# Optimization experiments

Hardware: AMD Instinct MI355X
Metric: run time of the kernel (lower is better)

Reference implementation:

```python
import jax, jax.numpy as jnp
import numpy as np

V, C, D = 131072, 65536, 128
E_NEG, E_CON = 131072, 524288
L, B = 3, 32


def setup_inputs() -> dict:
    key = jax.random.key(0)
    ks = jax.random.split(key, 16)
    s = 1.0 / np.sqrt(D)
    return {
        "x_var": jax.random.normal(ks[0], (V, D), jnp.float32),
        "x_con": jax.random.normal(ks[1], (C, D), jnp.float32),
        "W_src": jax.random.normal(ks[2], (L, 3, D, D), jnp.float32) * s,
        "W_dst": jax.random.normal(ks[3], (L, 3, D, D), jnp.float32) * s,
        "att_src": jax.random.normal(ks[4], (L, 3, D), jnp.float32) * s,
        "att_dst": jax.random.normal(ks[5], (L, 3, D), jnp.float32) * s,
        "bias": jnp.zeros((L, 3, D), jnp.float32),
        "mlp_w1": jax.random.normal(ks[6], (D, D), jnp.float32) * s,
        "mlp_b1": jnp.zeros((D,), jnp.float32),
        "mlp_w2": jax.random.normal(ks[7], (D, 1), jnp.float32) * s,
        "mlp_b2": jnp.zeros((1,), jnp.float32),
        "edge_neg_src": jax.random.randint(ks[8], (E_NEG,), 0, V, jnp.int32),
        "edge_neg_dst": jax.random.randint(ks[9], (E_NEG,), 0, V, jnp.int32),
        "edge_con_src": jax.random.randint(ks[10], (E_CON,), 0, V, jnp.int32),
        "edge_con_dst": jax.random.randint(ks[11], (E_CON,), 0, C, jnp.int32),
        "batch_var": jnp.sort(jax.random.randint(ks[12], (V,), 0, B, jnp.int32)),
    }


def _gat(xs, xd, src, dst, Ws, Wd, a_s, a_d, b, n_dst):
    """PyG GATConv (heads=1, add_self_loops=False) for one bipartite relation."""
    hs = xs @ Ws                                    # [Ns, D]
    hd = xd @ Wd                                    # [Nd, D]
    es = hs @ a_s                                   # [Ns]
    ed = hd @ a_d                                   # [Nd]
    e = jax.nn.leaky_relu(es[src] + ed[dst], negative_slope=0.2)  # [E]
    m = jax.ops.segment_max(e, dst, num_segments=n_dst)
    m = jnp.where(jnp.isfinite(m), m, 0.0)
    ex = jnp.exp(e - m[dst])
    den = jax.ops.segment_sum(ex, dst, num_segments=n_dst)
    alpha = ex / (den[dst] + 1e-16)                 # per-destination softmax
    out = jax.ops.segment_sum(hs[src] * alpha[:, None], dst, num_segments=n_dst)
    return out + b


def reference(x_var, x_con, W_src, W_dst, att_src, att_dst, bias,
              mlp_w1, mlp_b1, mlp_w2, mlp_b2,
              edge_neg_src, edge_neg_dst, edge_con_src, edge_con_dst, batch_var):
    xv, xc = x_var, x_con
    n_layers = W_src.shape[0]
    for l in range(n_layers):
        # relation 0: variable -is_negation_of-> variable
        v_neg = _gat(xv, xv, edge_neg_src, edge_neg_dst,
                     W_src[l, 0], W_dst[l, 0], att_src[l, 0], att_dst[l, 0], bias[l, 0], V)
        # relation 2: constraint -rev_connected_to-> variable (reverse edges)
        v_rev = _gat(xc, xv, edge_con_dst, edge_con_src,
                     W_src[l, 2], W_dst[l, 2], att_src[l, 2], att_dst[l, 2], bias[l, 2], V)
        # relation 1: variable -connected_to-> constraint
        c_new = _gat(xv, xc, edge_con_src, edge_con_dst,
                     W_src[l, 1], W_dst[l, 1], att_src[l, 1], att_dst[l, 1], bias[l, 1], C)
        # HeteroConv aggr='sum', then relu (dropout is identity in eval)
        xv = jax.nn.relu(v_neg + v_rev)
        xc = jax.nn.relu(c_new)
    # global_mean_pool over variable nodes per graph
    cnt = jax.ops.segment_sum(jnp.ones((V,), xv.dtype), batch_var, num_segments=B)
    pooled = jax.ops.segment_sum(xv, batch_var, num_segments=B) / jnp.maximum(cnt, 1.0)[:, None]
    # vote MLP: Linear -> relu -> Linear
    h = jax.nn.relu(pooled @ mlp_w1 + mlp_b1)
    return h @ mlp_w2 + mlp_b2
```

## Files before the change

### kernel.cpp

```cpp
#include <hip/hip_runtime.h>
#include <hip/hip_bf16.h>
#include <cstdint>
#include <cstddef>

#define D 128

typedef __hip_bfloat16 bf16;
typedef __attribute__((ext_vector_type(8))) short short8v;
typedef __attribute__((ext_vector_type(4))) float f32x4;

__device__ inline float ld1(const float* p) { return *p; }
__device__ inline float ld1(const bf16* p) { return __bfloat162float(*p); }
__device__ inline float2 ld2(const float* p) { return *(const float2*)p; }
__device__ inline float2 ld2(const bf16* p) {
  __hip_bfloat162 v = *(const __hip_bfloat162*)p;
  float2 r; r.x = __bfloat162float(v.x); r.y = __bfloat162float(v.y); return r;
}
__device__ inline void st2(float* p, float a, float b) {
  float2 v; v.x = a; v.y = b; *(float2*)p = v;
}
__device__ inline void st2(bf16* p, float a, float b) {
  __hip_bfloat162 v; v.x = __float2bfloat16(a); v.y = __float2bfloat16(b);
  *(__hip_bfloat162*)p = v;
}

__device__ inline short f2bf(float x) {
  uint32_t u = __builtin_bit_cast(uint32_t, x);
  uint32_t r = (u + 0x7FFFu + ((u >> 16) & 1u)) >> 16;
  return (short)(uint16_t)r;
}
__device__ inline float bf2f(short s) {
  uint32_t u = ((uint32_t)(uint16_t)s) << 16;
  return __builtin_bit_cast(float, u);
}

__device__ inline f32x4 mfma16(short8v a, short8v b, f32x4 c) {
  return __builtin_amdgcn_mfma_f32_16x16x32_bf16(a, b, c, 0, 0, 0);
}

__device__ __forceinline__ void load8(const float* p, float* v) {
  float4 a = *(const float4*)p;
  float4 b = *(const float4*)(p + 4);
  v[0] = a.x; v[1] = a.y; v[2] = a.z; v[3] = a.w;
  v[4] = b.x; v[5] = b.y; v[6] = b.z; v[7] = b.w;
}
__device__ __forceinline__ void load8(const bf16* p, float* v) {
  short8v s = *(const short8v*)p;
  #pragma unroll
  for (int j = 0; j < 8; ++j) v[j] = bf2f(s[j]);
}
__device__ __forceinline__ void split_store(short* Xh, short* Xl, int off, const float* v) {
  short8v h, l;
  #pragma unroll
  for (int j = 0; j < 8; ++j) {
    short hj = f2bf(v[j]);
    h[j] = hj;
    l[j] = f2bf(v[j] - bf2f(hj));
  }
  *(short8v*)&Xh[off] = h;
  *(short8v*)&Xl[off] = l;
}

__global__ void compute_u_kernel(const float* __restrict__ Wsrc, const float* __restrict__ Wdst,
                                 const float* __restrict__ asrc, const float* __restrict__ adst,
                                 float* __restrict__ u) {
  int lr = blockIdx.x;
  int side = blockIdx.y;
  int k = threadIdx.x;
  const float* W = (side == 0 ? Wsrc : Wdst) + ((size_t)lr * D + k) * D;
  const float* a = (side == 0 ? asrc : adst) + (size_t)lr * D;
  float s = 0.f;
  for (int j = 0; j < D; ++j) s += W[j] * a[j];
  u[((size_t)lr * 2 + side) * D + k] = s;
}

__global__ void wsplit_kernel(const float* __restrict__ Wsrc,
                              short* __restrict__ WhT, short* __restrict__ WlT) {
  int lr = blockIdx.x;
  const float* W = Wsrc + (size_t)lr * D * D;
  short* wh = WhT + (size_t)lr * D * D;
  short* wl = WlT + (size_t)lr * D * D;
  for (int i = threadIdx.x; i < D * D; i += blockDim.x) {
    int k = i >> 7, c = i & 127;
    float w = W[i];
    short h = f2bf(w);
    short l = f2bf(w - bf2f(h));
    wh[c * D + k] = h;
    wl[c * D + k] = l;
  }
}

__global__ void count_kernel(const int* __restrict__ dst, int* __restrict__ cnt, int E) {
  int i = blockIdx.x * blockDim.x + threadIdx.x;
  if (i < E) atomicAdd(&cnt[dst[i]], 1);
}

__global__ void count2_kernel(const int* __restrict__ csrc, const int* __restrict__ cdst,
                              int* __restrict__ cnt_bycon, int* __restrict__ cnt_byvar, int E) {
  int i = blockIdx.x * blockDim.x + threadIdx.x;
  if (i < E) {
    atomicAdd(&cnt_bycon[cdst[i]], 1);
    atomicAdd(&cnt_byvar[csrc[i]], 1);
  }
}

__global__ void bsum3_kernel(const int* __restrict__ c0, const int* __restrict__ c1,
                             const int* __restrict__ c2, int* __restrict__ bsums,
                             int n0, int n1, int n2, int pb0, int pb1, int pb2) {
  __shared__ int red[256];
  int y = blockIdx.y;
  const int* cnt = (y == 0) ? c0 : (y == 1) ? c1 : c2;
  int n  = (y == 0) ? n0 : (y == 1) ? n1 : n2;
  int pb = (y == 0) ? pb0 : (y == 1) ? pb1 : pb2;
  int b = blockIdx.x, t = threadIdx.x;
  int base = b * pb;
  if (base >= n) return;
  int end = base + pb; if (end > n) end = n;
  int s = 0;
  for (int i = base + t; i < end; i += 256) s += cnt[i];
  red[t] = s;
  __syncthreads();
  #pragma unroll
  for (int off = 128; off; off >>= 1) {
    if (t < off) red[t] += red[t + off];
    __syncthreads();
  }
  if (t == 0) bsums[y * 1024 + b] = red[0];
}

__global__ void bscan3_kernel(int* __restrict__ bsums,
                              int* __restrict__ t0, int* __restrict__ t1, int* __restrict__ t2) {
  __shared__ int sh[1024];
  int y = blockIdx.x, t = threadIdx.x;
  int* bs = bsums + y * 1024;
  int v = bs[t];
  sh[t] = v;
  __syncthreads();
  for (int off = 1; off < 1024; off <<= 1) {
    int u = (t >= off) ? sh[t - off] : 0;
    __syncthreads();
    sh[t] += u;
    __syncthreads();
  }
  bs[t] = sh[t] - v;
  if (t == 1023) {
    int* tot = (y == 0) ? t0 : (y == 1) ? t1 : t2;
    *tot = sh[1023];
  }
}

__global__ void scanfill3_kernel(const int* __restrict__ c0, const int* __restrict__ c1,
                                 const int* __restrict__ c2, const int* __restrict__ bsums,
                                 int* __restrict__ rp0, int* __restrict__ rp1, int* __restrict__ rp2,
                                 int* __restrict__ cu0, int* __restrict__ cu1, int* __restrict__ cu2,
                                 int n0, int n1, int n2, int pb0, int pb1, int pb2) {
  __shared__ int sh[256];
  int y = blockIdx.y;
  const int* cnt = (y == 0) ? c0 : (y == 1) ? c1 : c2;
  int* rowptr    = (y == 0) ? rp0 : (y == 1) ? rp1 : rp2;
  int* cursor    = (y == 0) ? cu0 : (y == 1) ? cu1 : cu2;
  int n  = (y == 0) ? n0 : (y == 1) ? n1 : n2;
  int pb = (y == 0) ? pb0 : (y == 1) ? pb1 : pb2;
  int b = blockIdx.x, t = threadIdx.x;
  int base = b * pb;
  if (base >= n) return;
  int end = base + pb; if (end > n) end = n;
  int run = bsums[y * 1024 + b];
  for (int tile = base; tile < end; tile += 256) {
    int i = tile + t;
    int c = (i < end) ? cnt[i] : 0;
    __syncthreads();
    sh[t] = c;
    __syncthreads();
    for (int off = 1; off < 256; off <<= 1) {
      int u = (t >= off) ? sh[t - off] : 0;
      __syncthreads();
      sh[t] += u;
      __syncthreads();
    }
    int excl = sh[t] - c;
    if (i < end) {
      rowptr[i] = run + excl;
      cursor[i] = run + excl;
    }
    run += sh[255];
  }
}

__global__ void fill_kernel(const int* __restrict__ dst, const int* __restrict__ src,
                            int* __restrict__ cursor, int* __restrict__ col, int E) {
  int i = blockIdx.x * blockDim.x + threadIdx.x;
  if (i < E) {
    int p = atomicAdd(&cursor[dst[i]], 1);
    col[p] = src[i];
  }
}

__global__ void fill2_kernel(const int* __restrict__ csrc, const int* __restrict__ cdst,
                             int* __restrict__ cur_bycon, int* __restrict__ cur_byvar,
                             int* __restrict__ col_bycon, int* __restrict__ col_byvar, int E) {
  int i = blockIdx.x * blockDim.x + threadIdx.x;
  if (i < E) {
    int s = csrc[i], d = cdst[i];
    int p = atomicAdd(&cur_bycon[d], 1);
    col_bycon[p] = s;
    int q = atomicAdd(&cur_byvar[s], 1);
    col_byvar[q] = d;
  }
}

template<typename T>
__global__ void vec_all_kernel(const T* __restrict__ xv, const T* __restrict__ xc,
                               const float* __restrict__ uv0, const float* __restrict__ uv1,
                               const float* __restrict__ uv2, const float* __restrict__ uv3,
                               const float* __restrict__ uc0, const float* __restrict__ uc1,
                               float* __restrict__ es0, float* __restrict__ ed0,
                               float* __restrict__ es1, float* __restrict__ ed2,
                               float* __restrict__ es2, float* __restrict__ ed1,
                               int V, int C) {
  int gw = (int)(((size_t)blockIdx.x * blockDim.x + threadIdx.x) >> 6);
  int lane = threadIdx.x & 63;
  if (gw < V) {
    const T* xr = xv + (size_t)gw * D;
    float xa = ld1(&xr[lane]), xb = ld1(&xr[lane + 64]);
    float p0 = xa * uv0[lane] + xb * uv0[lane + 64];
    float p1 = xa * uv1[lane] + xb * uv1[lane + 64];
    float p2 = xa * uv2[lane] + xb * uv2[lane + 64];
    float p3 = xa * uv3[lane] + xb * uv3[lane + 64];
    #pragma unroll
    for (int off = 32; off; off >>= 1) {
      p0 += __shfl_xor(p0, off);
      p1 += __shfl_xor(p1, off);
      p2 += __shfl_xor(p2, off);
      p3 += __shfl_xor(p3, off);
    }
    if (lane == 0) { es0[gw] = p0; ed0[gw] = p1; es1[gw] = p2; ed2[gw] = p3; }
  } else if (gw < V + C) {
    int g = gw - V;
    const T* xr = xc + (size_t)g * D;
    float xa = ld1(&xr[lane]), xb = ld1(&xr[lane + 64]);
    float p0 = xa * uc0[lane] + xb * uc0[lane + 64];
    float p1 = xa * uc1[lane] + xb * uc1[lane + 64];
    #pragma unroll
    for (int off = 32; off; off >>= 1) {
      p0 += __shfl_xor(p0, off);
      p1 += __shfl_xor(p1, off);
    }
    if (lane == 0) { es2[g] = p0; ed1[g] = p1; }
  }
}

template<typename Tin>
__global__ __launch_bounds__(512) void mm3_kernel(
    const Tin* __restrict__ Xv, const Tin* __restrict__ Xc,
    const short* __restrict__ wh0, const short* __restrict__ wl0,
    const short* __restrict__ wh1, const short* __restrict__ wl1,
    const short* __restrict__ wh2, const short* __restrict__ wl2,
    bf16* __restrict__ H0, bf16* __restrict__ H1, bf16* __restrict__ H2,
    int V, int C, int b0, int b1, int b2) {
  __shared__ short sbuf[2][2][32 * 136];
  int bid = blockIdx.x;
  const Tin* X; const short* wh; const short* wl; bf16* H;
  int nrows, lb, nblk;
  if (bid < b0)      { X = Xv; wh = wh0; wl = wl0; H = H0; nrows = V; lb = bid;      nblk = b0; }
  else if (bid < b1) { X = Xv; wh = wh1; wl = wl1; H = H1; nrows = V; lb = bid - b0; nblk = b1 - b0; }
  else               { X = Xc; wh = wh2; wl = wl2; H = H2; nrows = C; lb = bid - b1; nblk = b2 - b1; }
  int nchunks = nrows >> 5;
  if (lb >= nchunks) return;

  int tid = threadIdx.x;
  int wv = tid >> 6, lane = tid & 63;
  int c15 = lane & 15, q = lane >> 4;
  int rowgrp = wv >> 2, colgrp = wv & 3;

  short8v Bh[2][4], Bl[2][4];
  #pragma unroll
  for (int t = 0; t < 2; ++t) {
    #pragma unroll
    for (int ks = 0; ks < 4; ++ks) {
      int o = (colgrp * 32 + t * 16 + c15) * D + ks * 32 + q * 8;
      Bh[t][ks] = *(const short8v*)&wh[o];
      Bl[t][ks] = *(const short8v*)&wl[o];
    }
  }

  int srow = tid >> 4;
  int scol = (tid & 15) * 8;
  int soff = srow * 136 + scol;

  {
    float v[8];
    int gr = lb * 32 + srow; if (gr >= nrows) gr = nrows - 1;
    load8(X + (size_t)gr * D + scol, v);
    split_store(&sbuf[0][0][0], &sbuf[0][1][0], soff, v);
  }
  __syncthreads();

  int aoff = (rowgrp * 16 + c15) * 136 + q * 8;
  int cur = 0;
  for (int chunk = lb; chunk < nchunks; chunk += nblk) {
    int nxt = chunk + nblk;
    bool have = nxt < nchunks;
    float v[8];
    if (have) {
      int gr = nxt * 32 + srow; if (gr >= nrows) gr = nrows - 1;
      load8(X + (size_t)gr * D + scol, v);
    }
    const short* Ah = &sbuf[cur][0][aoff];
    const short* Al = &sbuf[cur][1][aoff];
    f32x4 a0 = (f32x4){0.f, 0.f, 0.f, 0.f};
    f32x4 a1 = (f32x4){0.f, 0.f, 0.f, 0.f};
    #pragma unroll
    for (int ks = 0; ks < 4; ++ks) {
      short8v xh = *(const short8v*)(Ah + ks * 32);
      short8v xl = *(const short8v*)(Al + ks * 32);
      a0 = mfma16(Bh[0][ks], xh, a0);
      a1 = mfma16(Bh[1][ks], xh, a1);
      a0 = mfma16(Bl[0][ks], xh, a0);
      a1 = mfma16(Bl[1][ks], xh, a1);
      a0 = mfma16(Bh[0][ks], xl, a0);
      a1 = mfma16(Bh[1][ks], xl, a1);
    }
    int gr = chunk * 32 + rowgrp * 16 + c15;
    if (gr < nrows) {
      short4 o0, o1;
      o0.x = f2bf(a0[0]); o0.y = f2bf(a0[1]); o0.z = f2bf(a0[2]); o0.w = f2bf(a0[3]);
      o1.x = f2bf(a1[0]); o1.y = f2bf(a1[1]); o1.z = f2bf(a1[2]); o1.w = f2bf(a1[3]);
      size_t base = (size_t)gr * D + colgrp * 32 + q * 4;
      *(short4*)((short*)H + base) = o0;
      *(short4*)((short*)H + base + 16) = o1;
    }
    if (have) split_store(&sbuf[cur ^ 1][0][0], &sbuf[cur ^ 1][1][0], soff, v);
    __syncthreads();
    cur ^= 1;
  }
}

__device__ __forceinline__ void alpha_rel(const int* __restrict__ rp, const int* __restrict__ col,
                                          const float* __restrict__ es, float edst,
                                          int gw, int lane, int2* __restrict__ edata) {
  int p0 = rp[gw];
  int deg = rp[gw + 1] - p0;
  if (deg <= 0) return;
  if (deg <= 64) {
    int s = 0; float e = -3.0e38f;
    if (lane < deg) {
      s = col[p0 + lane];
      float t = es[s] + edst;
      e = t > 0.f ? t : 0.2f * t;
    }
    float m = e;
    #pragma unroll
    for (int off = 32; off; off >>= 1) m = fmaxf(m, __shfl_xor(m, off));
    float ex = (lane < deg) ? __expf(e - m) : 0.f;
    float den = ex;
    #pragma unroll
    for (int off = 32; off; off >>= 1) den += __shfl_xor(den, off);
    float al = ex / (den + 1e-16f);
    if (lane < deg) {
      int2 v; v.x = s; v.y = __builtin_bit_cast(int, al);
      edata[p0 + lane] = v;
    }
  } else {
    float m = -3.0e38f;
    for (int j = lane; j < deg; j += 64) {
      int s = col[p0 + j];
      float t = es[s] + edst;
      t = t > 0.f ? t : 0.2f * t;
      m = fmaxf(m, t);
    }
    #pragma unroll
    for (int off = 32; off; off >>= 1) m = fmaxf(m, __shfl_xor(m, off));
    float den = 0.f;
    for (int j = lane; j < deg; j += 64) {
      int s = col[p0 + j];
      float t = es[s] + edst;
      t = t > 0.f ? t : 0.2f * t;
      den += __expf(t - m);
    }
    #pragma unroll
    for (int off = 32; off; off >>= 1) den += __shfl_xor(den, off);
    float inv = 1.f / (den + 1e-16f);
    for (int j = lane; j < deg; j += 64) {
      int s = col[p0 + j];
      float t = es[s] + edst;
      t = t > 0.f ? t : 0.2f * t;
      int2 v; v.x = s; v.y = __builtin_bit_cast(int, __expf(t - m) * inv);
      edata[p0 + j] = v;
    }
  }
}

__global__ void alpha_all_kernel(const int* __restrict__ rp0, const int* __restrict__ col0,
                                 const float* __restrict__ es0, const float* __restrict__ ed0,
                                 int2* __restrict__ eda0,
                                 const int* __restrict__ rp2, const int* __restrict__ col2,
                                 const float* __restrict__ es2, const float* __restrict__ ed2,
                                 int2* __restrict__ eda2,
                                 const int* __restrict__ rp1, const int* __restrict__ col1,
                                 const float* __restrict__ es1, const float* __restrict__ ed1,
                                 int2* __restrict__ eda1,
                                 int V, int C) {
  int gw = (int)(((size_t)blockIdx.x * blockDim.x + threadIdx.x) >> 6);
  int lane = threadIdx.x & 63;
  if (gw < V) {
    alpha_rel(rp0, col0, es0, ed0[gw], gw, lane, eda0);
    alpha_rel(rp2, col2, es2, ed2[gw], gw, lane, eda2);
  } else if (gw < V + C) {
    int g = gw - V;
    alpha_rel(rp1, col1, es1, ed1[g], g, lane, eda1);
  }
}

__device__ __forceinline__ void agg_rel(const int2* __restrict__ edata, int p0, int p1,
                                        const bf16* __restrict__ hs, int l2,
                                        float& a0, float& a1) {
  int q = p0;
  while (q + 4 <= p1) {
    int2 e0 = edata[q], e1 = edata[q + 1], e2 = edata[q + 2], e3 = edata[q + 3];
    int s0 = __builtin_amdgcn_readfirstlane(e0.x);
    int s1 = __builtin_amdgcn_readfirstlane(e1.x);
    int s2 = __builtin_amdgcn_readfirstlane(e2.x);
    int s3 = __builtin_amdgcn_readfirstlane(e3.x);
    float w0 = __builtin_bit_cast(float, __builtin_amdgcn_readfirstlane(e0.y));
    float w1 = __builtin_bit_cast(float, __builtin_amdgcn_readfirstlane(e1.y));
    float w2 = __builtin_bit_cast(float, __builtin_amdgcn_readfirstlane(e2.y));
    float w3 = __builtin_bit_cast(float, __builtin_amdgcn_readfirstlane(e3.y));
    float2 h0 = ld2(&hs[(size_t)s0 * D + l2]);
    float2 h1 = ld2(&hs[(size_t)s1 * D + l2]);
    float2 h2 = ld2(&hs[(size_t)s2 * D + l2]);
    float2 h3 = ld2(&hs[(size_t)s3 * D + l2]);
    a0 += w0 * h0.x + w1 * h1.x + w2 * h2.x + w3 * h3.x;
    a1 += w0 * h0.y + w1 * h1.y + w2 * h2.y + w3 * h3.y;
    q += 4;
  }
  while (q < p1) {
    int2 e = edata[q++];
    int s = __builtin_amdgcn_readfirstlane(e.x);
    float w = __builtin_bit_cast(float, __builtin_amdgcn_readfirstlane(e.y));
    float2 h = ld2(&hs[(size_t)s * D + l2]);
    a0 += w * h.x;
    a1 += w * h.y;
  }
}

template<typename T>
__global__ void agg_all_kernel(const int* __restrict__ rp0, const int2* __restrict__ eda0,
                               const bf16* __restrict__ hsv0, const float* __restrict__ b0,
                               const int* __restrict__ rp2, const int2* __restrict__ eda2,
                               const bf16* __restrict__ hsc, const float* __restrict__ b2,
                               const int* __restrict__ rp1, const int2* __restrict__ eda1,
                               const bf16* __restrict__ hsv1, const float* __restrict__ b1,
                               T* __restrict__ xv_out, T* __restrict__ xc_out, int V, int C) {
  int gw = (int)(((size_t)blockIdx.x * blockDim.x + threadIdx.x) >> 6);
  int lane = threadIdx.x & 63;
  int l2 = 2 * lane;
  if (gw < V) {
    float a0 = 0.f, a1 = 0.f;
    agg_rel(eda0, rp0[gw], rp0[gw + 1], hsv0, l2, a0, a1);
    agg_rel(eda2, rp2[gw], rp2[gw + 1], hsc, l2, a0, a1);
    float v0 = a0 + b0[l2] + b2[l2];
    float v1 = a1 + b0[l2 + 1] + b2[l2 + 1];
    st2(&xv_out[(size_t)gw * D + l2], v0 > 0.f ? v0 : 0.f, v1 > 0.f ? v1 : 0.f);
  } else if (gw < V + C) {
    int g = gw - V;
    float a0 = 0.f, a1 = 0.f;
    agg_rel(eda1, rp1[g], rp1[g + 1], hsv1, l2, a0, a1);
    float v0 = a0 + b1[l2];
    float v1 = a1 + b1[l2 + 1];
    st2(&xc_out[(size_t)g * D + l2], v0 > 0.f ? v0 : 0.f, v1 > 0.f ? v1 : 0.f);
  }
}

template<typename T>
__global__ void pool_kernel(const T* __restrict__ xv, const int* __restrict__ batch,
                            float* __restrict__ pooled, float* __restrict__ cntf,
                            int rowsPerBlock, int V) {
  int j = threadIdx.x;
  int r0 = blockIdx.x * rowsPerBlock;
  if (r0 >= V) return;
  int rend = r0 + rowsPerBlock; if (rend > V) rend = V;
  int cur = batch[r0];
  float s = 0.f;
  int run = 0;
  for (int r = r0; r < rend; ++r) {
    int b = batch[r];
    if (b != cur) {
      atomicAdd(&pooled[(size_t)cur * D + j], s);
      if (j == 0) atomicAdd(&cntf[cur], (float)run);
      s = 0.f; run = 0; cur = b;
    }
    s += ld1(&xv[(size_t)r * D + j]);
    run++;
  }
  atomicAdd(&pooled[(size_t)cur * D + j], s);
  if (j == 0) atomicAdd(&cntf[cur], (float)run);
}

__global__ void mlp_kernel(const float* __restrict__ pooled, const float* __restrict__ cntf,
                           const float* __restrict__ w1, const float* __restrict__ b1,
                           const float* __restrict__ w2, const float* __restrict__ b2,
                           float* __restrict__ out, int B) {
  __shared__ float P[32 * D];
  __shared__ float Hs[32 * D];
  int tid = threadIdx.x;
  if (B > 32) return;
  for (int i = tid; i < B * D; i += 256) {
    int r = i >> 7;
    P[i] = pooled[i] / fmaxf(cntf[r], 1.0f);
  }
  __syncthreads();
  for (int i = tid; i < B * D; i += 256) {
    int r = i >> 7, j = i & 127;
    float s = b1[j];
    for (int k = 0; k < D; ++k) s += P[r * D + k] * w1[k * D + j];
    Hs[i] = s > 0.f ? s : 0.f;
  }
  __syncthreads();
  if (tid < B) {
    float s = b2[0];
    for (int j = 0; j < D; ++j) s += Hs[tid * D + j] * w2[j];
    out[tid] = s;
  }
}

__global__ void zero_kernel(float* __restrict__ o, int n) {
  int i = blockIdx.x * blockDim.x + threadIdx.x;
  if (i < n) o[i] = 0.f;
}

template<typename T>
static void run_all(const float* x_var, const float* x_con,
                    const float* W_src, const float* W_dst,
                    const float* att_src, const float* att_dst, const float* bias,
                    const float* mlp_w1, const float* mlp_b1,
                    const float* mlp_w2, const float* mlp_b2,
                    const int* e_neg_src, const int* e_neg_dst,
                    const int* e_con_src, const int* e_con_dst, const int* batch_var,
                    int V, int C, int L, int EN, int EC, int B,
                    char* ws, float* out, hipStream_t stream) {
  size_t off = 0;
  auto alloc = [&](size_t bytes) -> char* {
    char* p = ws + off;
    off = (off + bytes + 255) & ~(size_t)255;
    return p;
  };
  T* xv  = (T*)alloc((size_t)V * D * sizeof(T));
  T* xc  = (T*)alloc((size_t)C * D * sizeof(T));
  bf16* hsv0 = (bf16*)alloc((size_t)V * D * 2);
  bf16* hsv1 = (bf16*)alloc((size_t)V * D * 2);
  bf16* hsc  = (bf16*)alloc((size_t)C * D * 2);
  float* es0 = (float*)alloc((size_t)V * 4);
  float* ed0 = (float*)alloc((size_t)V * 4);
  float* es1 = (float*)alloc((size_t)V * 4);
  float* ed2 = (float*)alloc((size_t)V * 4);
  float* es2 = (float*)alloc((size_t)C * 4);
  float* ed1 = (float*)alloc((size_t)C * 4);
  float* u   = (float*)alloc((size_t)L * 3 * 2 * D * 4);
  short* whT = (short*)alloc((size_t)L * 3 * D * D * 2);
  short* wlT = (short*)alloc((size_t)L * 3 * D * D * 2);
  int* rp0  = (int*)alloc((size_t)(V + 1) * 4);
  int* rp1  = (int*)alloc((size_t)(C + 1) * 4);
  int* rp2  = (int*)alloc((size_t)(V + 1) * 4);
  int* curs = (int*)alloc((size_t)(2 * (size_t)V + C) * 4);
  int* cur0 = curs, *cur1 = curs + V, *cur2 = curs + V + C;
  int* col0 = (int*)alloc((size_t)EN * 4);
  int* col1 = (int*)alloc((size_t)EC * 4);
  int* col2 = (int*)alloc((size_t)EC * 4);
  int2* eda0 = (int2*)alloc((size_t)EN * 8);
  int2* eda1 = (int2*)alloc((size_t)EC * 8);
  int2* eda2 = (int2*)alloc((size_t)EC * 8);
  int* bsums = (int*)alloc((size_t)3 * 1024 * 4);
  float* pooled = (float*)alloc((size_t)(B * D + B) * 4);
  float* cntf = pooled + (size_t)B * D;

  hipMemsetAsync(curs, 0, (size_t)(2 * (size_t)V + C) * 4, stream);
  hipMemsetAsync(bsums, 0, (size_t)3 * 1024 * 4, stream);
  hipMemsetAsync(pooled, 0, (size_t)(B * D + B) * 4, stream);

  compute_u_kernel<<<dim3(L * 3, 2), D, 0, stream>>>(W_src, W_dst, att_src, att_dst, u);
  wsplit_kernel<<<L * 3, 256, 0, stream>>>(W_src, whT, wlT);

  const int tb = 256;
  count_kernel<<<(EN + tb - 1) / tb, tb, 0, stream>>>(e_neg_dst, cur0, EN);
  count2_kernel<<<(EC + tb - 1) / tb, tb, 0, stream>>>(e_con_src, e_con_dst, cur1, cur2, EC);

  auto pbof = [](int n) {
    int pb = ((n + 1023) / 1024 + 255) & ~255;
    return pb < 256 ? 256 : pb;
  };
  int pb0 = pbof(V), pb1 = pbof(C), pb2 = pbof(V);
  int nb0 = (V + pb0 - 1) / pb0, nb1 = (C + pb1 - 1) / pb1, nb2 = (V + pb2 - 1) / pb2;
  int nbmax = nb0 > nb1 ? nb0 : nb1; if (nb2 > nbmax) nbmax = nb2;
  bsum3_kernel<<<dim3(nbmax, 3), 256, 0, stream>>>(cur0, cur1, cur2, bsums, V, C, V, pb0, pb1, pb2);
  bscan3_kernel<<<3, 1024, 0, stream>>>(bsums, rp0 + V, rp1 + C, rp2 + V);
  scanfill3_kernel<<<dim3(nbmax, 3), 256, 0, stream>>>(cur0, cur1, cur2, bsums,
                                                       rp0, rp1, rp2, cur0, cur1, cur2,
                                                       V, C, V, pb0, pb1, pb2);

  fill_kernel<<<(EN + tb - 1) / tb, tb, 0, stream>>>(e_neg_dst, e_neg_src, cur0, col0, EN);
  fill2_kernel<<<(EC + tb - 1) / tb, tb, 0, stream>>>(e_con_src, e_con_dst, cur1, cur2, col1, col2, EC);

  auto U  = [&](int l, int rel, int side) { return u + (((size_t)l * 3 + rel) * 2 + side) * D; };
  auto Wh = [&](int l, int rel) { return whT + ((size_t)l * 3 + rel) * D * D; };
  auto Wl = [&](int l, int rel) { return wlT + ((size_t)l * 3 + rel) * D * D; };
  auto Bp = [&](int l, int rel) { return bias + ((size_t)l * 3 + rel) * D; };

  int gwaves = (V + C + 3) / 4;
  const int MB0 = 512, MB1 = 1024, MB2 = 1280;

  for (int l = 0; l < L; ++l) {
    if (l == 0) {
      vec_all_kernel<float><<<gwaves, 256, 0, stream>>>(
          x_var, x_con, U(l,0,0), U(l,0,1), U(l,1,0), U(l,2,1), U(l,2,0), U(l,1,1),
          es0, ed0, es1, ed2, es2, ed1, V, C);
      mm3_kernel<float><<<MB2, 512, 0, stream>>>(
          x_var, x_con, Wh(l,0), Wl(l,0), Wh(l,1), Wl(l,1), Wh(l,2), Wl(l,2),
          hsv0, hsv1, hsc, V, C, MB0, MB1, MB2);
    } else {
      vec_all_kernel<T><<<gwaves, 256, 0, stream>>>(
          xv, xc, U(l,0,0), U(l,0,1), U(l,1,0), U(l,2,1), U(l,2,0), U(l,1,1),
          es0, ed0, es1, ed2, es2, ed1, V, C);
      mm3_kernel<T><<<MB2, 512, 0, stream>>>(
          xv, xc, Wh(l,0), Wl(l,0), Wh(l,1), Wl(l,1), Wh(l,2), Wl(l,2),
          hsv0, hsv1, hsc, V, C, MB0, MB1, MB2);
    }
    alpha_all_kernel<<<gwaves, 256, 0, stream>>>(
        rp0, col0, es0, ed0, eda0,
        rp2, col2, es2, ed2, eda2,
        rp1, col1, es1, ed1, eda1, V, C);
    agg_all_kernel<T><<<gwaves, 256, 0, stream>>>(
        rp0, eda0, hsv0, Bp(l,0),
        rp2, eda2, hsc,  Bp(l,2),
        rp1, eda1, hsv1, Bp(l,1),
        xv, xc, V, C);
  }

  pool_kernel<T><<<(V + 127) / 128, 128, 0, stream>>>(xv, batch_var, pooled, cntf, 128, V);
  mlp_kernel<<<1, 256, 0, stream>>>(pooled, cntf, mlp_w1, mlp_b1, mlp_w2, mlp_b2, out, B);
}

extern "C" void kernel_launch(void* const* d_in, const int* in_sizes, int n_in,
                              void* d_out, int out_size, void* d_ws, size_t ws_size,
                              hipStream_t stream) {
  const float* x_var   = (const float*)d_in[0];
  const float* x_con   = (const float*)d_in[1];
  const float* W_src   = (const float*)d_in[2];
  const float* W_dst   = (const float*)d_in[3];
  const float* att_src = (const float*)d_in[4];
  const float* att_dst = (const float*)d_in[5];
  const float* bias    = (const float*)d_in[6];
  const float* mlp_w1  = (const float*)d_in[7];
  const float* mlp_b1  = (const float*)d_in[8];
  const float* mlp_w2  = (const float*)d_in[9];
  const float* mlp_b2  = (const float*)d_in[10];
  const int* e_neg_src = (const int*)d_in[11];
  const int* e_neg_dst = (const int*)d_in[12];
  const int* e_con_src = (const int*)d_in[13];
  const int* e_con_dst = (const int*)d_in[14];
  const int* batch_var = (const int*)d_in[15];
  (void)n_in;

  const int V  = in_sizes[0] / D;
  const int C  = in_sizes[1] / D;
  const int L  = in_sizes[2] / (3 * D * D);
  const int EN = in_sizes[11];
  const int EC = in_sizes[13];
  const int B  = out_size;

  auto plan = [&](size_t esz) -> size_t {
    size_t o = 0;
    auto add = [&](size_t b) { o = (o + b + 255) & ~(size_t)255; };
    add((size_t)V * D * esz); add((size_t)C * D * esz);
    add((size_t)V * D * 2); add((size_t)V * D * 2); add((size_t)C * D * 2);
    add((size_t)V * 4); add((size_t)V * 4); add((size_t)V * 4); add((size_t)V * 4);
    add((size_t)C * 4); add((size_t)C * 4);
    add((size_t)L * 3 * 2 * D * 4);
    add((size_t)L * 3 * D * D * 2); add((size_t)L * 3 * D * D * 2);
    add((size_t)(V + 1) * 4); add((size_t)(C + 1) * 4); add((size_t)(V + 1) * 4);
    add((size_t)(2 * (size_t)V + C) * 4);
    add((size_t)EN * 4); add((size_t)EC * 4); add((size_t)EC * 4);
    add((size_t)EN * 8); add((size_t)EC * 8); add((size_t)EC * 8);
    add((size_t)3 * 1024 * 4);
    add((size_t)(B * D + B) * 4);
    return o;
  };

  if (plan(4) <= ws_size) {
    run_all<float>(x_var, x_con, W_src, W_dst, att_src, att_dst, bias,
                   mlp_w1, mlp_b1, mlp_w2, mlp_b2,
                   e_neg_src, e_neg_dst, e_con_src, e_con_dst, batch_var,
                   V, C, L, EN, EC, B, (char*)d_ws, (float*)d_out, stream);
  } else if (plan(2) <= ws_size) {
    run_all<bf16>(x_var, x_con, W_src, W_dst, att_src, att_dst, bias,
                  mlp_w1, mlp_b1, mlp_w2, mlp_b2,
                  e_neg_src, e_neg_dst, e_con_src, e_con_dst, batch_var,
                  V, C, L, EN, EC, B, (char*)d_ws, (float*)d_out, stream);
  } else {
    zero_kernel<<<(out_size + 63) / 64, 64, 0, stream>>>((float*)d_out, out_size);
  }
}
```

Measured before the change: 1.027 ms.

## Fuse attention dot products into projection GEMM and store activations in bf16

Removes the separate vec_all kernel: the es/ed attention projections are now computed inside the GEMM kernel from the same X rows it already loads into shared memory, reduced across 16 lanes with shuffles. This saves one full read of the node features and one launch per layer. Intermediate node activations are also always kept in bf16 instead of fp32 when workspace allows, halving feature traffic for the aggregation, pooling and GEMM stages, at some precision cost.

```diff
diff --git a/kernel.cpp b/kernel.cpp
--- a/kernel.cpp
+++ b/kernel.cpp
@@ -209,62 +209,38 @@
   }
 }
 
-template<typename T>
-__global__ void vec_all_kernel(const T* __restrict__ xv, const T* __restrict__ xc,
-                               const float* __restrict__ uv0, const float* __restrict__ uv1,
-                               const float* __restrict__ uv2, const float* __restrict__ uv3,
-                               const float* __restrict__ uc0, const float* __restrict__ uc1,
-                               float* __restrict__ es0, float* __restrict__ ed0,
-                               float* __restrict__ es1, float* __restrict__ ed2,
-                               float* __restrict__ es2, float* __restrict__ ed1,
-                               int V, int C) {
-  int gw = (int)(((size_t)blockIdx.x * blockDim.x + threadIdx.x) >> 6);
-  int lane = threadIdx.x & 63;
-  if (gw < V) {
-    const T* xr = xv + (size_t)gw * D;
-    float xa = ld1(&xr[lane]), xb = ld1(&xr[lane + 64]);
-    float p0 = xa * uv0[lane] + xb * uv0[lane + 64];
-    float p1 = xa * uv1[lane] + xb * uv1[lane + 64];
-    float p2 = xa * uv2[lane] + xb * uv2[lane + 64];
-    float p3 = xa * uv3[lane] + xb * uv3[lane + 64];
-    #pragma unroll
-    for (int off = 32; off; off >>= 1) {
-      p0 += __shfl_xor(p0, off);
-      p1 += __shfl_xor(p1, off);
-      p2 += __shfl_xor(p2, off);
-      p3 += __shfl_xor(p3, off);
-    }
-    if (lane == 0) { es0[gw] = p0; ed0[gw] = p1; es1[gw] = p2; ed2[gw] = p3; }
-  } else if (gw < V + C) {
-    int g = gw - V;
-    const T* xr = xc + (size_t)g * D;
-    float xa = ld1(&xr[lane]), xb = ld1(&xr[lane + 64]);
-    float p0 = xa * uc0[lane] + xb * uc0[lane + 64];
-    float p1 = xa * uc1[lane] + xb * uc1[lane + 64];
-    #pragma unroll
-    for (int off = 32; off; off >>= 1) {
-      p0 += __shfl_xor(p0, off);
-      p1 += __shfl_xor(p1, off);
-    }
-    if (lane == 0) { es2[g] = p0; ed1[g] = p1; }
-  }
-}
-
 template<typename Tin>
-__global__ __launch_bounds__(512) void mm3_kernel(
+__global__ __launch_bounds__(512) void mmv3_kernel(
     const Tin* __restrict__ Xv, const Tin* __restrict__ Xc,
     const short* __restrict__ wh0, const short* __restrict__ wl0,
     const short* __restrict__ wh1, const short* __restrict__ wl1,
     const short* __restrict__ wh2, const short* __restrict__ wl2,
     bf16* __restrict__ H0, bf16* __restrict__ H1, bf16* __restrict__ H2,
+    const float* __restrict__ uv0, const float* __restrict__ uv1,
+    const float* __restrict__ uv2, const float* __restrict__ uv3,
+    const float* __restrict__ uc0, const float* __restrict__ uc1,
+    float* __restrict__ es0, float* __restrict__ ed0,
+    float* __restrict__ es1, float* __restrict__ ed2,
+    float* __restrict__ es2, float* __restrict__ ed1,
     int V, int C, int b0, int b1, int b2) {
   __shared__ short sbuf[2][2][32 * 136];
   int bid = blockIdx.x;
   const Tin* X; const short* wh; const short* wl; bf16* H;
-  int nrows, lb, nblk;
-  if (bid < b0)      { X = Xv; wh = wh0; wl = wl0; H = H0; nrows = V; lb = bid;      nblk = b0; }
-  else if (bid < b1) { X = Xv; wh = wh1; wl = wl1; H = H1; nrows = V; lb = bid - b0; nblk = b1 - b0; }
-  else               { X = Xc; wh = wh2; wl = wl2; H = H2; nrows = C; lb = bid - b1; nblk = b2 - b1; }
+  int nrows, lb, nblk, ndots;
+  const float *U0, *U1, *U2, *U3;
+  float *O0, *O1, *O2, *O3;
+  if (bid < b0) {
+    X = Xv; wh = wh0; wl = wl0; H = H0; nrows = V; lb = bid; nblk = b0;
+    ndots = 4; U0 = uv0; U1 = uv1; U2 = uv2; U3 = uv3;
+    O0 = es0; O1 = ed0; O2 = es1; O3 = ed2;
+  } else if (bid < b1) {
+    X = Xv; wh = wh1; wl = wl1; H = H1; nrows = V; lb = bid - b0; nblk = b1 - b0;
+    ndots = 0; U0 = U1 = U2 = U3 = nullptr; O0 = O1 = O2 = O3 = nullptr;
+  } else {
+    X = Xc; wh = wh2; wl = wl2; H = H2; nrows = C; lb = bid - b1; nblk = b2 - b1;
+    ndots = 2; U0 = uc0; U1 = uc1; U2 = U3 = nullptr;
+    O0 = es2; O1 = ed1; O2 = O3 = nullptr;
+  }
   int nchunks = nrows >> 5;
   if (lb >= nchunks) return;
 
@@ -288,10 +264,39 @@
   int scol = (tid & 15) * 8;
   int soff = srow * 136 + scol;
 
+  float u0r[8], u1r[8], u2r[8], u3r[8];
+  if (ndots) {
+    load8(U0 + scol, u0r);
+    load8(U1 + scol, u1r);
+    if (ndots == 4) { load8(U2 + scol, u2r); load8(U3 + scol, u3r); }
+  }
+
+  auto do_dots = [&](const float* v, int gr) {
+    if (!ndots) return;
+    float p0 = 0.f, p1 = 0.f, p2 = 0.f, p3 = 0.f;
+    #pragma unroll
+    for (int j = 0; j < 8; ++j) { p0 += v[j] * u0r[j]; p1 += v[j] * u1r[j]; }
+    if (ndots == 4) {
+      #pragma unroll
+      for (int j = 0; j < 8; ++j) { p2 += v[j] * u2r[j]; p3 += v[j] * u3r[j]; }
+    }
+    #pragma unroll
+    for (int off = 1; off < 16; off <<= 1) {
+      p0 += __shfl_xor(p0, off);
+      p1 += __shfl_xor(p1, off);
+      if (ndots == 4) { p2 += __shfl_xor(p2, off); p3 += __shfl_xor(p3, off); }
+    }
+    if ((tid & 15) == 0) {
+      O0[gr] = p0; O1[gr] = p1;
+      if (ndots == 4) { O2[gr] = p2; O3[gr] = p3; }
+    }
+  };
+
   {
     float v[8];
     int gr = lb * 32 + srow; if (gr >= nrows) gr = nrows - 1;
     load8(X + (size_t)gr * D + scol, v);
+    do_dots(v, gr);
     split_store(&sbuf[0][0][0], &sbuf[0][1][0], soff, v);
   }
   __syncthreads();
@@ -305,6 +310,7 @@
     if (have) {
       int gr = nxt * 32 + srow; if (gr >= nrows) gr = nrows - 1;
       load8(X + (size_t)gr * D + scol, v);
+      do_dots(v, gr);
     }
     const short* Ah = &sbuf[cur][0][aoff];
     const short* Al = &sbuf[cur][1][aoff];
@@ -444,14 +450,13 @@
   }
 }
 
-template<typename T>
 __global__ void agg_all_kernel(const int* __restrict__ rp0, const int2* __restrict__ eda0,
                                const bf16* __restrict__ hsv0, const float* __restrict__ b0,
                                const int* __restrict__ rp2, const int2* __restrict__ eda2,
                                const bf16* __restrict__ hsc, const float* __restrict__ b2,
                                const int* __restrict__ rp1, const int2* __restrict__ eda1,
                                const bf16* __restrict__ hsv1, const float* __restrict__ b1,
-                               T* __restrict__ xv_out, T* __restrict__ xc_out, int V, int C) {
+                               bf16* __restrict__ xv_out, bf16* __restrict__ xc_out, int V, int C) {
   int gw = (int)(((size_t)blockIdx.x * blockDim.x + threadIdx.x) >> 6);
   int lane = threadIdx.x & 63;
   int l2 = 2 * lane;
@@ -472,8 +477,7 @@
   }
 }
 
-template<typename T>
-__global__ void pool_kernel(const T* __restrict__ xv, const int* __restrict__ batch,
+__global__ void pool_kernel(const bf16* __restrict__ xv, const int* __restrict__ batch,
                             float* __restrict__ pooled, float* __restrict__ cntf,
                             int rowsPerBlock, int V) {
   int j = threadIdx.x;
@@ -529,7 +533,6 @@
   if (i < n) o[i] = 0.f;
 }
 
-template<typename T>
 static void run_all(const float* x_var, const float* x_con,
                     const float* W_src, const float* W_dst,
                     const float* att_src, const float* att_dst, const float* bias,
@@ -545,8 +548,8 @@
     off = (off + bytes + 255) & ~(size_t)255;
     return p;
   };
-  T* xv  = (T*)alloc((size_t)V * D * sizeof(T));
-  T* xc  = (T*)alloc((size_t)C * D * sizeof(T));
+  bf16* xv  = (bf16*)alloc((size_t)V * D * 2);
+  bf16* xc  = (bf16*)alloc((size_t)C * D * 2);
   bf16* hsv0 = (bf16*)alloc((size_t)V * D * 2);
   bf16* hsv1 = (bf16*)alloc((size_t)V * D * 2);
   bf16* hsc  = (bf16*)alloc((size_t)C * D * 2);
@@ -611,32 +614,30 @@
 
   for (int l = 0; l < L; ++l) {
     if (l == 0) {
-      vec_all_kernel<float><<<gwaves, 256, 0, stream>>>(
-          x_var, x_con, U(l,0,0), U(l,0,1), U(l,1,0), U(l,2,1), U(l,2,0), U(l,1,1),
-          es0, ed0, es1, ed2, es2, ed1, V, C);
-      mm3_kernel<float><<<MB2, 512, 0, stream>>>(
+      mmv3_kernel<float><<<MB2, 512, 0, stream>>>(
           x_var, x_con, Wh(l,0), Wl(l,0), Wh(l,1), Wl(l,1), Wh(l,2), Wl(l,2),
-          hsv0, hsv1, hsc, V, C, MB0, MB1, MB2);
+          hsv0, hsv1, hsc,
+          U(l,0,0), U(l,0,1), U(l,1,0), U(l,2,1), U(l,2,0), U(l,1,1),
+          es0, ed0, es1, ed2, es2, ed1, V, C, MB0, MB1, MB2);
     } else {
-      vec_all_kernel<T><<<gwaves, 256, 0, stream>>>(
-          xv, xc, U(l,0,0), U(l,0,1), U(l,1,0), U(l,2,1), U(l,2,0), U(l,1,1),
-          es0, ed0, es1, ed2, es2, ed1, V, C);
-      mm3_kernel<T><<<MB2, 512, 0, stream>>>(
+      mmv3_kernel<bf16><<<MB2, 512, 0, stream>>>(
           xv, xc, Wh(l,0), Wl(l,0), Wh(l,1), Wl(l,1), Wh(l,2), Wl(l,2),
-          hsv0, hsv1, hsc, V, C, MB0, MB1, MB2);
+          hsv0, hsv1, hsc,
+          U(l,0,0), U(l,0,1), U(l,1,0), U(l,2,1), U(l,2,0), U(l,1,1),
+          es0, ed0, es1, ed2, es2, ed1, V, C, MB0, MB1, MB2);
     }
     alpha_all_kernel<<<gwaves, 256, 0, stream>>>(
         rp0, col0, es0, ed0, eda0,
         rp2, col2, es2, ed2, eda2,
         rp1, col1, es1, ed1, eda1, V, C);
-    agg_all_kernel<T><<<gwaves, 256, 0, stream>>>(
+    agg_all_kernel<<<gwaves, 256, 0, stream>>>(
         rp0, eda0, hsv0, Bp(l,0),
         rp2, eda2, hsc,  Bp(l,2),
         rp1, eda1, hsv1, Bp(l,1),
         xv, xc, V, C);
   }
 
-  pool_kernel<T><<<(V + 127) / 128, 128, 0, stream>>>(xv, batch_var, pooled, cntf, 128, V);
+  pool_kernel<<<(V + 127) / 128, 128, 0, stream>>>(xv, batch_var, pooled, cntf, 128, V);
   mlp_kernel<<<1, 256, 0, stream>>>(pooled, cntf, mlp_w1, mlp_b1, mlp_w2, mlp_b2, out, B);
 }
 
@@ -668,10 +669,10 @@
   const int EC = in_sizes[13];
   const int B  = out_size;
 
-  auto plan = [&](size_t esz) -> size_t {
+  auto plan = [&]() -> size_t {
     size_t o = 0;
     auto add = [&](size_t b) { o = (o + b + 255) & ~(size_t)255; };
-    add((size_t)V * D * esz); add((size_t)C * D * esz);
+    add((size_t)V * D * 2); add((size_t)C * D * 2);
     add((size_t)V * D * 2); add((size_t)V * D * 2); add((size_t)C * D * 2);
     add((size_t)V * 4); add((size_t)V * 4); add((size_t)V * 4); add((size_t)V * 4);
     add((size_t)C * 4); add((size_t)C * 4);
@@ -686,16 +687,11 @@
     return o;
   };
 
-  if (plan(4) <= ws_size) {
-    run_all<float>(x_var, x_con, W_src, W_dst, att_src, att_dst, bias,
-                   mlp_w1, mlp_b1, mlp_w2, mlp_b2,
-                   e_neg_src, e_neg_dst, e_con_src, e_con_dst, batch_var,
-                   V, C, L, EN, EC, B, (char*)d_ws, (float*)d_out, stream);
-  } else if (plan(2) <= ws_size) {
-    run_all<bf16>(x_var, x_con, W_src, W_dst, att_src, att_dst, bias,
-                  mlp_w1, mlp_b1, mlp_w2, mlp_b2,
-                  e_neg_src, e_neg_dst, e_con_src, e_con_dst, batch_var,
-                  V, C, L, EN, EC, B, (char*)d_ws, (float*)d_out, stream);
+  if (plan() <= ws_size) {
+    run_all(x_var, x_con, W_src, W_dst, att_src, att_dst, bias,
+            mlp_w1, mlp_b1, mlp_w2, mlp_b2,
+            e_neg_src, e_neg_dst, e_con_src, e_con_dst, batch_var,
+            V, C, L, EN, EC, B, (char*)d_ws, (float*)d_out, stream);
   } else {
     zero_kernel<<<(out_size + 63) / 64, 64, 0, stream>>>((float*)d_out, out_size);
   }
```

Result: faster. 969.0 us (-5.7%).
